# Optimization experiments

Measured on AMD Instinct MI355X. Metric: run time of the kernel, lower is better.

## Reference

```python
import jax, jax.numpy as jnp
import numpy as np

N = 100_000      # nodes
E = 800_000      # edges (avg degree 8)
D_IN = 16        # embedding_dimension
H = 128          # hidden_dimension
OUT = 3          # out_dim
NEG_SLOPE = 0.01 # LeakyReLU default


def setup_inputs() -> dict:
    key = jax.random.key(0)
    ks = jax.random.split(key, 9)
    s = 0.05
    return {
        "feature": jax.random.normal(ks[0], (N, D_IN), jnp.float32),
        "edge_index": jax.random.randint(ks[1], (2, E), 0, N, dtype=jnp.int64),
        "edge_type": jax.random.randint(ks[2], (E,), 0, 2, dtype=jnp.int64),
        "W_in": jax.random.normal(ks[3], (D_IN, H), jnp.float32) * s,
        "b_in": jnp.zeros((H,), jnp.float32),
        "W1": jax.random.normal(ks[4], (H, H), jnp.float32) * s,
        "b1": jnp.zeros((H,), jnp.float32),
        "W2": jax.random.normal(ks[5], (H, H), jnp.float32) * s,
        "b2": jnp.zeros((H,), jnp.float32),
        "W_out": jax.random.normal(ks[6], (H, OUT), jnp.float32) * s,
        "b_out": jnp.zeros((OUT,), jnp.float32),
    }


def gcn_conv(x, W, b, src, dst, n):
    """PyG GCNConv: linear -> add self-loops -> D^-1/2 A D^-1/2 aggregation -> bias."""
    h = x @ W                                   # [N, H]
    loop = jnp.arange(n, dtype=src.dtype)
    src_sl = jnp.concatenate([src, loop])       # [E+N]
    dst_sl = jnp.concatenate([dst, loop])
    deg = jax.ops.segment_sum(jnp.ones_like(dst_sl, dtype=h.dtype), dst_sl, num_segments=n)
    dinv = jax.lax.rsqrt(jnp.maximum(deg, 1.0))  # deg >= 1 due to self-loops
    norm = dinv[src_sl] * dinv[dst_sl]          # [E+N]
    msg = h[src_sl] * norm[:, None]             # gather + scale, [E+N, H]
    out = jax.ops.segment_sum(msg, dst_sl, num_segments=n)  # scatter-add
    return out + b


def reference(feature, edge_index, edge_type, W_in, b_in, W1, b1, W2, b2, W_out, b_out):
    # edge_type is accepted but unused, exactly as in the torch forward.
    x = jax.nn.leaky_relu(feature.astype(jnp.float32) @ W_in + b_in, NEG_SLOPE)
    src, dst = edge_index[0], edge_index[1]
    x = gcn_conv(x, W1, b1, src, dst, N)
    # F.dropout with training=False is identity (inference path)
    x = gcn_conv(x, W2, b2, src, dst, N)
    return x @ W_out + b_out
```

## Files before the change

### kernel.cpp

```cpp
#include <hip/hip_runtime.h>
#include <hip/hip_bf16.h>
#include <cstdint>

#define DIN 16
#define HD  128
#define RNG 2048
#define LB  11
#define MAXB 64
#define PB  256

static __device__ __forceinline__ void fma4(float4& a, float s, const float4 v) {
    a.x = fmaf(s, v.x, a.x);
    a.y = fmaf(s, v.y, a.y);
    a.z = fmaf(s, v.z, a.z);
    a.w = fmaf(s, v.w, a.w);
}
static __device__ __forceinline__ void add4(float4& a, const float4 v) {
    a.x += v.x; a.y += v.y; a.z += v.z; a.w += v.w;
}
static __device__ __forceinline__ void lrelu4(float4& h) {
    h.x = h.x > 0.f ? h.x : 0.01f * h.x;
    h.y = h.y > 0.f ? h.y : 0.01f * h.y;
    h.z = h.z > 0.f ? h.z : 0.01f * h.z;
    h.w = h.w > 0.f ? h.w : 0.01f * h.w;
}

__global__ __launch_bounds__(256) void k_histfold(const int* __restrict__ dst,
                                                  int* __restrict__ hist,
                                                  int E, int R, int CHK,
                                                  const float* __restrict__ W1,
                                                  const float* __restrict__ b1,
                                                  const float* __restrict__ W2,
                                                  const float* __restrict__ b2,
                                                  const float* __restrict__ Wout,
                                                  const float* __restrict__ bout,
                                                  float* __restrict__ Wcp,
                                                  float* __restrict__ cbuf) {
    int tid = threadIdx.x;
    if (blockIdx.x < PB) {
        __shared__ int h[MAXB];
        for (int i = tid; i < R; i += 256) h[i] = 0;
        __syncthreads();
        int e0 = blockIdx.x * CHK;
        int e1 = e0 + CHK; if (e1 > E) e1 = E;
        for (int e = e0 + tid; e < e1; e += 256) atomicAdd(&h[dst[e] >> LB], 1);
        __syncthreads();
        for (int i = tid; i < R; i += 256) hist[i * PB + blockIdx.x] = h[i];
        return;
    }
    __shared__ float sT[HD * 3];
    for (int idx = tid; idx < HD * 3; idx += 256) {
        int k = idx / 3, o = idx - 3 * k;
        float s = 0.f;
        for (int j = 0; j < HD; j++) s = fmaf(W2[k * HD + j], Wout[j * 3 + o], s);
        sT[idx] = s;
    }
    if (tid < 3) {
        float s = bout[tid];
        for (int j = 0; j < HD; j++) s = fmaf(b2[j], Wout[j * 3 + tid], s);
        cbuf[3 + tid] = s;
    }
    __syncthreads();
    if (tid < 3) {
        float s = 0.f;
        for (int j = 0; j < HD; j++) s = fmaf(b1[j], sT[j * 3 + tid], s);
        cbuf[tid] = s;
    }
    for (int idx = tid; idx < HD * 3; idx += 256) {
        int k = idx / 3, o = idx - 3 * k;
        float s = 0.f;
        for (int j = 0; j < HD; j++) s = fmaf(W1[k * HD + j], sT[j * 3 + o], s);
        Wcp[k * 4 + o] = s;
    }
    for (int idx = tid; idx < HD; idx += 256) Wcp[idx * 4 + 3] = 0.f;
}

__global__ __launch_bounds__(1024) void k_scanmlp(int* __restrict__ hist, int nh,
                                                  const float* __restrict__ F,
                                                  const float* __restrict__ Win,
                                                  const float* __restrict__ bin,
                                                  const float4* __restrict__ Wcp,
                                                  float4* __restrict__ Y, int N) {
    int tid = threadIdx.x;
    if (blockIdx.x == 0) {
        __shared__ int sd[1024];
        int CH = (nh + 1023) / 1024;
        int c0 = tid * CH;
        int c1 = c0 + CH; if (c1 > nh) c1 = nh;
        int sum = 0;
        for (int i = c0; i < c1; i++) sum += hist[i];
        sd[tid] = sum;
        __syncthreads();
        for (int off = 1; off < 1024; off <<= 1) {
            int t = (tid >= off) ? sd[tid - off] : 0;
            __syncthreads();
            sd[tid] += t;
            __syncthreads();
        }
        int base = sd[tid] - sum;
        for (int i = c0; i < c1; i++) { int t = hist[i]; hist[i] = base; base += t; }
        return;
    }
    __shared__ float4 sWinT[DIN * HD / 4];
    __shared__ float4 sWcT[HD];
    __shared__ float4 sBin[HD / 4];
    __shared__ float  sF[128 * DIN];
    if (tid < DIN * HD / 4) {
        int k = tid >> 5, rem = tid & 31, l = rem >> 1, c = rem & 1;
        sWinT[k * 32 + c * 16 + l] = ((const float4*)Win)[tid];
    } else if (tid < DIN * HD / 4 + HD) {
        int i = tid - DIN * HD / 4;
        sWcT[(i & 7) * 16 + (i >> 3)] = Wcp[i];
    } else if (tid < DIN * HD / 4 + HD + HD / 4) {
        int i = tid - DIN * HD / 4 - HD;
        sBin[i] = ((const float4*)bin)[i];
    }
    int base = (blockIdx.x - 1) * 128;
    {
        int n0 = base + (tid >> 4);
        sF[tid] = (n0 < N) ? F[(size_t)base * DIN + tid] : 0.f;
        int n1 = base + ((tid + 1024) >> 4);
        sF[tid + 1024] = (n1 < N) ? F[(size_t)base * DIN + tid + 1024] : 0.f;
    }
    __syncthreads();
    int l = tid & 15;
    int g = tid >> 4;
    int nodeA = base + 2 * g;
    int nodeB = nodeA + 1;
    if (nodeA >= N) return;
    float4 a0 = sBin[l * 2 + 0], a1 = sBin[l * 2 + 1];
    float4 b0 = a0, b1 = a1;
    #pragma unroll
    for (int k = 0; k < DIN; k++) {
        float4 w0 = sWinT[k * 32 + l];
        float4 w1 = sWinT[k * 32 + 16 + l];
        float fA = sF[(2 * g) * DIN + k];
        float fB = sF[(2 * g + 1) * DIN + k];
        fma4(a0, fA, w0); fma4(a1, fA, w1);
        fma4(b0, fB, w0); fma4(b1, fB, w1);
    }
    lrelu4(a0); lrelu4(a1); lrelu4(b0); lrelu4(b1);
    float hA[8] = {a0.x, a0.y, a0.z, a0.w, a1.x, a1.y, a1.z, a1.w};
    float hB[8] = {b0.x, b0.y, b0.z, b0.w, b1.x, b1.y, b1.z, b1.w};
    float pA0 = 0.f, pA1 = 0.f, pA2 = 0.f, pB0 = 0.f, pB1 = 0.f, pB2 = 0.f;
    #pragma unroll
    for (int jj = 0; jj < 8; jj++) {
        float4 wc = sWcT[jj * 16 + l];
        pA0 = fmaf(hA[jj], wc.x, pA0);
        pA1 = fmaf(hA[jj], wc.y, pA1);
        pA2 = fmaf(hA[jj], wc.z, pA2);
        pB0 = fmaf(hB[jj], wc.x, pB0);
        pB1 = fmaf(hB[jj], wc.y, pB1);
        pB2 = fmaf(hB[jj], wc.z, pB2);
    }
    #pragma unroll
    for (int off = 8; off > 0; off >>= 1) {
        pA0 += __shfl_down(pA0, off, 16);
        pA1 += __shfl_down(pA1, off, 16);
        pA2 += __shfl_down(pA2, off, 16);
        pB0 += __shfl_down(pB0, off, 16);
        pB1 += __shfl_down(pB1, off, 16);
        pB2 += __shfl_down(pB2, off, 16);
    }
    if (l == 0) {
        Y[nodeA] = make_float4(pA0, pA1, pA2, 1.0f);
        if (nodeB < N) Y[nodeB] = make_float4(pB0, pB1, pB2, 1.0f);
    }
}

__global__ __launch_bounds__(256) void k_part(const int* __restrict__ src,
                                              const int* __restrict__ dst,
                                              const int* __restrict__ off,
                                              int* __restrict__ ebin,
                                              int E, int R, int CHK) {
    __shared__ int cur[MAXB];
    int tid = threadIdx.x;
    int b = blockIdx.x;
    for (int i = tid; i < R; i += 256) cur[i] = off[i * PB + b];
    __syncthreads();
    int e0 = b * CHK;
    int e1 = e0 + CHK; if (e1 > E) e1 = E;
    for (int e = e0 + tid; e < e1; e += 256) {
        int s = src[e], d = dst[e];
        int pos = atomicAdd(&cur[d >> LB], 1);
        ebin[pos] = (s << LB) | (d & (RNG - 1));
    }
}

__global__ __launch_bounds__(1024) void k_csr(const int* __restrict__ ebin,
                                              const int* __restrict__ off,
                                              const float4* __restrict__ Y,
                                              int* __restrict__ rowptr,
                                              int* __restrict__ ecsr,
                                              float* __restrict__ dinv,
                                              float4* __restrict__ Ys,
                                              int N, int E, int R) {
    __shared__ int c[RNG];
    __shared__ int swv[16];
    int tid = threadIdx.x;
    int b = blockIdx.x;
    c[tid] = 0; c[tid + 1024] = 0;
    __syncthreads();
    int e0 = off[b * PB];
    int e1 = (b + 1 < R) ? off[(b + 1) * PB] : E;
    for (int e = e0 + tid; e < e1; e += 1024) atomicAdd(&c[ebin[e] & (RNG - 1)], 1);
    __syncthreads();
    int v0 = c[2 * tid], v1 = c[2 * tid + 1];
    int ts = v0 + v1;
    int lane = tid & 63, wid = tid >> 6;
    int sc = ts;
    #pragma unroll
    for (int o = 1; o < 64; o <<= 1) {
        int t = __shfl_up(sc, o, 64);
        if (lane >= o) sc += t;
    }
    if (lane == 63) swv[wid] = sc;
    __syncthreads();
    if (tid < 16) {
        int v = swv[tid];
        int s2 = v;
        #pragma unroll
        for (int o = 1; o < 16; o <<= 1) {
            int t = __shfl_up(s2, o, 16);
            if (tid >= o) s2 += t;
        }
        swv[tid] = s2 - v;
    }
    __syncthreads();
    int excl = sc - ts + swv[wid];
    int rp0 = e0 + excl;
    int rp1 = rp0 + v0;
    int n0 = b * RNG + 2 * tid;
    if (n0 <= N) rowptr[n0] = rp0;
    if (n0 + 1 <= N) rowptr[n0 + 1] = rp1;
    if (b == R - 1 && tid == 1023) rowptr[N] = E;
    if (n0 < N) {
        float di = rsqrtf((float)v0 + 1.0f);
        dinv[n0] = di;
        float4 y = Y[n0];
        Ys[n0] = make_float4(di * y.x, di * y.y, di * y.z, di);
    }
    if (n0 + 1 < N) {
        float di = rsqrtf((float)v1 + 1.0f);
        dinv[n0 + 1] = di;
        float4 y = Y[n0 + 1];
        Ys[n0 + 1] = make_float4(di * y.x, di * y.y, di * y.z, di);
    }
    c[2 * tid] = rp0;
    c[2 * tid + 1] = rp1;
    __syncthreads();
    for (int e = e0 + tid; e < e1; e += 1024) {
        int ed = ebin[e];
        int pos = atomicAdd(&c[ed & (RNG - 1)], 1);
        ecsr[pos] = ed >> LB;
    }
    if (b == 0 && tid < 16) ecsr[E + tid] = 0;
}

__global__ __launch_bounds__(256) void k_aggA(const int* __restrict__ rowptr,
                                              const int* __restrict__ ecsr,
                                              const float4* __restrict__ Ys,
                                              const float* __restrict__ dinv,
                                              float4* __restrict__ Z1s, int N) {
    int n = blockIdx.x * blockDim.x + threadIdx.x;
    if (n >= N) return;
    int beg = rowptr[n], end = rowptr[n + 1];
    int deg = end - beg;
    float4 acc = Ys[n];
    int4 q0 = *(const int4*)(ecsr + beg);
    int4 q1 = *(const int4*)(ecsr + beg + 4);
    int4 q2 = *(const int4*)(ecsr + beg + 8);
    int si[12] = {q0.x, q0.y, q0.z, q0.w, q1.x, q1.y, q1.z, q1.w,
                  q2.x, q2.y, q2.z, q2.w};
    float4 g[12];
    #pragma unroll
    for (int k = 0; k < 12; k++) g[k] = Ys[si[k]];
    #pragma unroll
    for (int k = 0; k < 12; k++) if (k < deg) add4(acc, g[k]);
    for (int j = beg + 12; j < end; j++) add4(acc, Ys[ecsr[j]]);
    float di = dinv[n];
    float d2 = di * di;
    Z1s[n] = make_float4(d2 * acc.x, d2 * acc.y, d2 * acc.z, d2 * acc.w);
}

__global__ __launch_bounds__(256) void k_aggB(const int* __restrict__ rowptr,
                                              const int* __restrict__ ecsr,
                                              const float4* __restrict__ Z1s,
                                              const float* __restrict__ dinv,
                                              const float* __restrict__ cbuf,
                                              float* __restrict__ out, int N) {
    int n = blockIdx.x * blockDim.x + threadIdx.x;
    if (n >= N) return;
    int beg = rowptr[n], end = rowptr[n + 1];
    int deg = end - beg;
    float4 acc = Z1s[n];
    float di = dinv[n];
    float r = acc.w / di;
    int4 q0 = *(const int4*)(ecsr + beg);
    int4 q1 = *(const int4*)(ecsr + beg + 4);
    int4 q2 = *(const int4*)(ecsr + beg + 8);
    int si[12] = {q0.x, q0.y, q0.z, q0.w, q1.x, q1.y, q1.z, q1.w,
                  q2.x, q2.y, q2.z, q2.w};
    float4 g[12];
    #pragma unroll
    for (int k = 0; k < 12; k++) g[k] = Z1s[si[k]];
    #pragma unroll
    for (int k = 0; k < 12; k++) if (k < deg) add4(acc, g[k]);
    for (int j = beg + 12; j < end; j++) add4(acc, Z1s[ecsr[j]]);
    out[(size_t)n * 3 + 0] = di * acc.x + r * cbuf[0] + cbuf[3];
    out[(size_t)n * 3 + 1] = di * acc.y + r * cbuf[1] + cbuf[4];
    out[(size_t)n * 3 + 2] = di * acc.z + r * cbuf[2] + cbuf[5];
}

extern "C" void kernel_launch(void* const* d_in, const int* in_sizes, int n_in,
                              void* d_out, int out_size, void* d_ws, size_t ws_size,
                              hipStream_t stream) {
    const float* feat = (const float*)d_in[0];
    const int*   ei   = (const int*)d_in[1];
    const float* Win  = (const float*)d_in[3];
    const float* bin  = (const float*)d_in[4];
    const float* W1   = (const float*)d_in[5];
    const float* b1   = (const float*)d_in[6];
    const float* W2   = (const float*)d_in[7];
    const float* b2   = (const float*)d_in[8];
    const float* Wout = (const float*)d_in[9];
    const float* bout = (const float*)d_in[10];
    float* out = (float*)d_out;

    int N = in_sizes[0] / DIN;
    int E = in_sizes[2];
    const int* src = ei;
    const int* dst = ei + E;

    int R = (N + RNG - 1) >> LB;
    int CHK = (E + PB - 1) / PB;
    int NH = R * PB;
    int XB = (N + 127) / 128;

    char* p = (char*)d_ws;
    auto alloc = [&](size_t bytes) -> char* {
        char* q = p;
        p += (bytes + 511) & ~(size_t)511;
        return q;
    };
    int*    hist   = (int*)alloc((size_t)NH * 4);
    int*    ebin   = (int*)alloc((size_t)E * 4);
    int*    ecsr   = (int*)alloc(((size_t)E + 16) * 4);
    int*    rowptr = (int*)alloc((size_t)(N + 1) * 4);
    float4* Y      = (float4*)alloc((size_t)N * 16);
    float4* Ys     = (float4*)alloc((size_t)N * 16);
    float4* Z1s    = (float4*)alloc((size_t)N * 16);
    float*  dinv   = (float*)alloc((size_t)N * 4);
    float*  Wcp    = (float*)alloc(HD * 4 * 4);
    float*  cbuf   = (float*)alloc(8 * 4);

    k_histfold<<<PB + 1, 256, 0, stream>>>(dst, hist, E, R, CHK,
                                           W1, b1, W2, b2, Wout, bout, Wcp, cbuf);
    k_scanmlp<<<1 + XB, 1024, 0, stream>>>(hist, NH, feat, Win, bin,
                                           (const float4*)Wcp, Y, N);
    k_part<<<PB, 256, 0, stream>>>(src, dst, hist, ebin, E, R, CHK);
    k_csr<<<R, 1024, 0, stream>>>(ebin, hist, Y, rowptr, ecsr, dinv, Ys, N, E, R);
    k_aggA<<<(N + 255) / 256, 256, 0, stream>>>(rowptr, ecsr, Ys, dinv, Z1s, N);
    k_aggB<<<(N + 255) / 256, 256, 0, stream>>>(rowptr, ecsr, Z1s, dinv, cbuf, out, N);
}
```

Baseline: 156.1 us.

## Replace histogram-scan edge partition with fixed-capacity bins and packed row descriptors

Drops the separate histogram and prefix-scan pass. Edges are now partitioned straight into fixed-capacity per-bin buffers, with global atomic cursors and block-local staging in shared memory. Row pointer and degree are packed into one int, so the dinv array goes away and the aggregation kernels recompute dinv with rsqrt. The folded weight product is recomputed in every MLP block and in the first CSR block, which removes one kernel launch but adds redundant per-block compute. Correctness now assumes each node's in-degree stays below 64 and that each bin fits its capacity.

```diff
diff --git a/kernel.cpp b/kernel.cpp
--- a/kernel.cpp
+++ b/kernel.cpp
@@ -7,7 +7,7 @@
 #define RNG 2048
 #define LB  11
 #define MAXB 64
-#define PB  256
+#define CHKE 3328
 
 static __device__ __forceinline__ void fma4(float4& a, float s, const float4 v) {
     a.x = fmaf(s, v.x, a.x);
@@ -25,102 +25,47 @@
     h.w = h.w > 0.f ? h.w : 0.01f * h.w;
 }
 
-__global__ __launch_bounds__(256) void k_histfold(const int* __restrict__ dst,
-                                                  int* __restrict__ hist,
-                                                  int E, int R, int CHK,
-                                                  const float* __restrict__ W1,
-                                                  const float* __restrict__ b1,
-                                                  const float* __restrict__ W2,
-                                                  const float* __restrict__ b2,
-                                                  const float* __restrict__ Wout,
-                                                  const float* __restrict__ bout,
-                                                  float* __restrict__ Wcp,
-                                                  float* __restrict__ cbuf) {
-    int tid = threadIdx.x;
-    if (blockIdx.x < PB) {
-        __shared__ int h[MAXB];
-        for (int i = tid; i < R; i += 256) h[i] = 0;
-        __syncthreads();
-        int e0 = blockIdx.x * CHK;
-        int e1 = e0 + CHK; if (e1 > E) e1 = E;
-        for (int e = e0 + tid; e < e1; e += 256) atomicAdd(&h[dst[e] >> LB], 1);
-        __syncthreads();
-        for (int i = tid; i < R; i += 256) hist[i * PB + blockIdx.x] = h[i];
-        return;
-    }
-    __shared__ float sT[HD * 3];
-    for (int idx = tid; idx < HD * 3; idx += 256) {
-        int k = idx / 3, o = idx - 3 * k;
-        float s = 0.f;
-        for (int j = 0; j < HD; j++) s = fmaf(W2[k * HD + j], Wout[j * 3 + o], s);
-        sT[idx] = s;
-    }
-    if (tid < 3) {
-        float s = bout[tid];
-        for (int j = 0; j < HD; j++) s = fmaf(b2[j], Wout[j * 3 + tid], s);
-        cbuf[3 + tid] = s;
-    }
-    __syncthreads();
-    if (tid < 3) {
-        float s = 0.f;
-        for (int j = 0; j < HD; j++) s = fmaf(b1[j], sT[j * 3 + tid], s);
-        cbuf[tid] = s;
-    }
-    for (int idx = tid; idx < HD * 3; idx += 256) {
-        int k = idx / 3, o = idx - 3 * k;
-        float s = 0.f;
-        for (int j = 0; j < HD; j++) s = fmaf(W1[k * HD + j], sT[j * 3 + o], s);
-        Wcp[k * 4 + o] = s;
-    }
-    for (int idx = tid; idx < HD; idx += 256) Wcp[idx * 4 + 3] = 0.f;
-}
-
-__global__ __launch_bounds__(1024) void k_scanmlp(int* __restrict__ hist, int nh,
-                                                  const float* __restrict__ F,
-                                                  const float* __restrict__ Win,
-                                                  const float* __restrict__ bin,
-                                                  const float4* __restrict__ Wcp,
-                                                  float4* __restrict__ Y, int N) {
-    int tid = threadIdx.x;
-    if (blockIdx.x == 0) {
-        __shared__ int sd[1024];
-        int CH = (nh + 1023) / 1024;
-        int c0 = tid * CH;
-        int c1 = c0 + CH; if (c1 > nh) c1 = nh;
-        int sum = 0;
-        for (int i = c0; i < c1; i++) sum += hist[i];
-        sd[tid] = sum;
-        __syncthreads();
-        for (int off = 1; off < 1024; off <<= 1) {
-            int t = (tid >= off) ? sd[tid - off] : 0;
-            __syncthreads();
-            sd[tid] += t;
-            __syncthreads();
-        }
-        int base = sd[tid] - sum;
-        for (int i = c0; i < c1; i++) { int t = hist[i]; hist[i] = base; base += t; }
-        return;
-    }
+__global__ __launch_bounds__(1024) void k_mlp(const float* __restrict__ F,
+                                              const float* __restrict__ Win,
+                                              const float* __restrict__ binp,
+                                              const float* __restrict__ W1,
+                                              const float* __restrict__ W2,
+                                              const float* __restrict__ Wout,
+                                              int* __restrict__ binCursor,
+                                              float4* __restrict__ Y, int N, int R) {
     __shared__ float4 sWinT[DIN * HD / 4];
     __shared__ float4 sWcT[HD];
     __shared__ float4 sBin[HD / 4];
     __shared__ float  sF[128 * DIN];
+    __shared__ float  sT[HD * 3];
+    int tid = threadIdx.x;
+    if (blockIdx.x == 0 && tid < R * 16) binCursor[tid] = 0;
     if (tid < DIN * HD / 4) {
         int k = tid >> 5, rem = tid & 31, l = rem >> 1, c = rem & 1;
         sWinT[k * 32 + c * 16 + l] = ((const float4*)Win)[tid];
-    } else if (tid < DIN * HD / 4 + HD) {
+    } else if (tid < DIN * HD / 4 + HD / 4) {
         int i = tid - DIN * HD / 4;
-        sWcT[(i & 7) * 16 + (i >> 3)] = Wcp[i];
-    } else if (tid < DIN * HD / 4 + HD + HD / 4) {
-        int i = tid - DIN * HD / 4 - HD;
-        sBin[i] = ((const float4*)bin)[i];
-    }
-    int base = (blockIdx.x - 1) * 128;
+        sBin[i] = ((const float4*)binp)[i];
+    }
+    int base = blockIdx.x * 128;
     {
         int n0 = base + (tid >> 4);
         sF[tid] = (n0 < N) ? F[(size_t)base * DIN + tid] : 0.f;
         int n1 = base + ((tid + 1024) >> 4);
         sF[tid + 1024] = (n1 < N) ? F[(size_t)base * DIN + tid + 1024] : 0.f;
+    }
+    if (tid < HD * 3) {
+        int k = tid / 3, o = tid - 3 * k;
+        float s = 0.f;
+        for (int j = 0; j < HD; j++) s = fmaf(W2[k * HD + j], Wout[j * 3 + o], s);
+        sT[tid] = s;
+    }
+    __syncthreads();
+    if (tid < HD * 3) {
+        int k = tid / 3, o = tid - 3 * k;
+        float s = 0.f;
+        for (int j = 0; j < HD; j++) s = fmaf(W1[k * HD + j], sT[j * 3 + o], s);
+        ((float*)&sWcT[(k & 7) * 16 + (k >> 3)])[o] = s;
     }
     __syncthreads();
     int l = tid & 15;
@@ -170,40 +115,78 @@
 
 __global__ __launch_bounds__(256) void k_part(const int* __restrict__ src,
                                               const int* __restrict__ dst,
-                                              const int* __restrict__ off,
+                                              int* __restrict__ binCursor,
                                               int* __restrict__ ebin,
-                                              int E, int R, int CHK) {
-    __shared__ int cur[MAXB];
+                                              int E, int R, int CAPE) {
+    __shared__ int sV[CHKE];
+    __shared__ unsigned char sB[CHKE];
+    __shared__ int lcnt[MAXB], lbase[MAXB];
     int tid = threadIdx.x;
-    int b = blockIdx.x;
-    for (int i = tid; i < R; i += 256) cur[i] = off[i * PB + b];
-    __syncthreads();
-    int e0 = b * CHK;
-    int e1 = e0 + CHK; if (e1 > E) e1 = E;
-    for (int e = e0 + tid; e < e1; e += 256) {
-        int s = src[e], d = dst[e];
-        int pos = atomicAdd(&cur[d >> LB], 1);
-        ebin[pos] = (s << LB) | (d & (RNG - 1));
+    if (tid < R) lcnt[tid] = 0;
+    __syncthreads();
+    int e0 = blockIdx.x * CHKE;
+    int cnt = E - e0; if (cnt > CHKE) cnt = CHKE;
+    for (int i = tid; i < cnt; i += 256) {
+        int s = src[e0 + i], d = dst[e0 + i];
+        int b = d >> LB;
+        sV[i] = (s << LB) | (d & (RNG - 1));
+        sB[i] = (unsigned char)b;
+        atomicAdd(&lcnt[b], 1);
+    }
+    __syncthreads();
+    if (tid < R) lbase[tid] = atomicAdd(&binCursor[tid * 16], lcnt[tid]);
+    __syncthreads();
+    if (tid < R) lcnt[tid] = lbase[tid];
+    __syncthreads();
+    for (int i = tid; i < cnt; i += 256) {
+        int b = sB[i];
+        int pos = atomicAdd(&lcnt[b], 1);
+        ebin[b * CAPE + pos] = sV[i];
     }
 }
 
 __global__ __launch_bounds__(1024) void k_csr(const int* __restrict__ ebin,
-                                              const int* __restrict__ off,
+                                              const int* __restrict__ binCursor,
                                               const float4* __restrict__ Y,
-                                              int* __restrict__ rowptr,
+                                              int* __restrict__ rowdeg,
                                               int* __restrict__ ecsr,
-                                              float* __restrict__ dinv,
                                               float4* __restrict__ Ys,
-                                              int N, int E, int R) {
+                                              const float* __restrict__ W2,
+                                              const float* __restrict__ Wout,
+                                              const float* __restrict__ b1,
+                                              const float* __restrict__ b2,
+                                              const float* __restrict__ bout,
+                                              float* __restrict__ cbuf,
+                                              int N, int R, int CAPE) {
     __shared__ int c[RNG];
     __shared__ int swv[16];
+    __shared__ float sTc[HD * 3];
     int tid = threadIdx.x;
     int b = blockIdx.x;
     c[tid] = 0; c[tid + 1024] = 0;
-    __syncthreads();
-    int e0 = off[b * PB];
-    int e1 = (b + 1 < R) ? off[(b + 1) * PB] : E;
+    if (b == 0 && tid < HD * 3) {
+        int k = tid / 3, o = tid - 3 * k;
+        float s = 0.f;
+        for (int j = 0; j < HD; j++) s = fmaf(W2[k * HD + j], Wout[j * 3 + o], s);
+        sTc[tid] = s;
+    }
+    if (b == 0 && tid >= HD * 3 && tid < HD * 3 + 3) {
+        int o = tid - HD * 3;
+        float s = bout[o];
+        for (int j = 0; j < HD; j++) s = fmaf(b2[j], Wout[j * 3 + o], s);
+        cbuf[3 + o] = s;
+    }
+    __syncthreads();
+    if (b == 0 && tid < 3) {
+        float s = 0.f;
+        for (int j = 0; j < HD; j++) s = fmaf(b1[j], sTc[j * 3 + tid], s);
+        cbuf[tid] = s;
+    }
+    int e0 = b * CAPE;
+    int cntb = binCursor[b * 16];
+    int e1 = e0 + cntb;
     for (int e = e0 + tid; e < e1; e += 1024) atomicAdd(&c[ebin[e] & (RNG - 1)], 1);
+    if (tid < 16) ecsr[e1 + tid] = 0;
     __syncthreads();
     int v0 = c[2 * tid], v1 = c[2 * tid + 1];
     int ts = v0 + v1;
@@ -231,18 +214,15 @@
     int rp0 = e0 + excl;
     int rp1 = rp0 + v0;
     int n0 = b * RNG + 2 * tid;
-    if (n0 <= N) rowptr[n0] = rp0;
-    if (n0 + 1 <= N) rowptr[n0 + 1] = rp1;
-    if (b == R - 1 && tid == 1023) rowptr[N] = E;
     if (n0 < N) {
+        rowdeg[n0] = (rp0 << 6) | v0;
         float di = rsqrtf((float)v0 + 1.0f);
-        dinv[n0] = di;
         float4 y = Y[n0];
         Ys[n0] = make_float4(di * y.x, di * y.y, di * y.z, di);
     }
     if (n0 + 1 < N) {
+        rowdeg[n0 + 1] = (rp1 << 6) | v1;
         float di = rsqrtf((float)v1 + 1.0f);
-        dinv[n0 + 1] = di;
         float4 y = Y[n0 + 1];
         Ys[n0 + 1] = make_float4(di * y.x, di * y.y, di * y.z, di);
     }
@@ -254,18 +234,16 @@
         int pos = atomicAdd(&c[ed & (RNG - 1)], 1);
         ecsr[pos] = ed >> LB;
     }
-    if (b == 0 && tid < 16) ecsr[E + tid] = 0;
-}
-
-__global__ __launch_bounds__(256) void k_aggA(const int* __restrict__ rowptr,
+}
+
+__global__ __launch_bounds__(256) void k_aggA(const int* __restrict__ rowdeg,
                                               const int* __restrict__ ecsr,
                                               const float4* __restrict__ Ys,
-                                              const float* __restrict__ dinv,
                                               float4* __restrict__ Z1s, int N) {
     int n = blockIdx.x * blockDim.x + threadIdx.x;
     if (n >= N) return;
-    int beg = rowptr[n], end = rowptr[n + 1];
-    int deg = end - beg;
+    int rd = rowdeg[n];
+    int beg = rd >> 6, deg = rd & 63;
     float4 acc = Ys[n];
     int4 q0 = *(const int4*)(ecsr + beg);
     int4 q1 = *(const int4*)(ecsr + beg + 4);
@@ -277,24 +255,23 @@
     for (int k = 0; k < 12; k++) g[k] = Ys[si[k]];
     #pragma unroll
     for (int k = 0; k < 12; k++) if (k < deg) add4(acc, g[k]);
-    for (int j = beg + 12; j < end; j++) add4(acc, Ys[ecsr[j]]);
-    float di = dinv[n];
+    for (int j = beg + 12; j < beg + deg; j++) add4(acc, Ys[ecsr[j]]);
+    float di = rsqrtf((float)deg + 1.0f);
     float d2 = di * di;
     Z1s[n] = make_float4(d2 * acc.x, d2 * acc.y, d2 * acc.z, d2 * acc.w);
 }
 
-__global__ __launch_bounds__(256) void k_aggB(const int* __restrict__ rowptr,
+__global__ __launch_bounds__(256) void k_aggB(const int* __restrict__ rowdeg,
                                               const int* __restrict__ ecsr,
                                               const float4* __restrict__ Z1s,
-                                              const float* __restrict__ dinv,
                                               const float* __restrict__ cbuf,
                                               float* __restrict__ out, int N) {
     int n = blockIdx.x * blockDim.x + threadIdx.x;
     if (n >= N) return;
-    int beg = rowptr[n], end = rowptr[n + 1];
-    int deg = end - beg;
+    int rd = rowdeg[n];
+    int beg = rd >> 6, deg = rd & 63;
+    float di = rsqrtf((float)deg + 1.0f);
     float4 acc = Z1s[n];
-    float di = dinv[n];
     float r = acc.w / di;
     int4 q0 = *(const int4*)(ecsr + beg);
     int4 q1 = *(const int4*)(ecsr + beg + 4);
@@ -306,7 +283,7 @@
     for (int k = 0; k < 12; k++) g[k] = Z1s[si[k]];
     #pragma unroll
     for (int k = 0; k < 12; k++) if (k < deg) add4(acc, g[k]);
-    for (int j = beg + 12; j < end; j++) add4(acc, Z1s[ecsr[j]]);
+    for (int j = beg + 12; j < beg + deg; j++) add4(acc, Z1s[ecsr[j]]);
     out[(size_t)n * 3 + 0] = di * acc.x + r * cbuf[0] + cbuf[3];
     out[(size_t)n * 3 + 1] = di * acc.y + r * cbuf[1] + cbuf[4];
     out[(size_t)n * 3 + 2] = di * acc.z + r * cbuf[2] + cbuf[5];
@@ -318,7 +295,7 @@
     const float* feat = (const float*)d_in[0];
     const int*   ei   = (const int*)d_in[1];
     const float* Win  = (const float*)d_in[3];
-    const float* bin  = (const float*)d_in[4];
+    const float* binp = (const float*)d_in[4];
     const float* W1   = (const float*)d_in[5];
     const float* b1   = (const float*)d_in[6];
     const float* W2   = (const float*)d_in[7];
@@ -333,9 +310,9 @@
     const int* dst = ei + E;
 
     int R = (N + RNG - 1) >> LB;
-    int CHK = (E + PB - 1) / PB;
-    int NH = R * PB;
+    int CAPE = (((E + R - 1) / R) + 2064) & ~15;
     int XB = (N + 127) / 128;
+    int PBn = (E + CHKE - 1) / CHKE;
 
     char* p = (char*)d_ws;
     auto alloc = [&](size_t bytes) -> char* {
@@ -343,23 +320,19 @@
         p += (bytes + 511) & ~(size_t)511;
         return q;
     };
-    int*    hist   = (int*)alloc((size_t)NH * 4);
-    int*    ebin   = (int*)alloc((size_t)E * 4);
-    int*    ecsr   = (int*)alloc(((size_t)E + 16) * 4);
-    int*    rowptr = (int*)alloc((size_t)(N + 1) * 4);
+    int*    binCursor = (int*)alloc((size_t)R * 16 * 4);
+    int*    ebin   = (int*)alloc((size_t)R * CAPE * 4);
+    int*    ecsr   = (int*)alloc(((size_t)R * CAPE + 16) * 4);
+    int*    rowdeg = (int*)alloc((size_t)N * 4);
     float4* Y      = (float4*)alloc((size_t)N * 16);
     float4* Ys     = (float4*)alloc((size_t)N * 16);
     float4* Z1s    = (float4*)alloc((size_t)N * 16);
-    float*  dinv   = (float*)alloc((size_t)N * 4);
-    float*  Wcp    = (float*)alloc(HD * 4 * 4);
     float*  cbuf   = (float*)alloc(8 * 4);
 
-    k_histfold<<<PB + 1, 256, 0, stream>>>(dst, hist, E, R, CHK,
-                                           W1, b1, W2, b2, Wout, bout, Wcp, cbuf);
-    k_scanmlp<<<1 + XB, 1024, 0, stream>>>(hist, NH, feat, Win, bin,
-                                           (const float4*)Wcp, Y, N);
-    k_part<<<PB, 256, 0, stream>>>(src, dst, hist, ebin, E, R, CHK);
-    k_csr<<<R, 1024, 0, stream>>>(ebin, hist, Y, rowptr, ecsr, dinv, Ys, N, E, R);
-    k_aggA<<<(N + 255) / 256, 256, 0, stream>>>(rowptr, ecsr, Ys, dinv, Z1s, N);
-    k_aggB<<<(N + 255) / 256, 256, 0, stream>>>(rowptr, ecsr, Z1s, dinv, cbuf, out, N);
-}
+    k_mlp<<<XB, 1024, 0, stream>>>(feat, Win, binp, W1, W2, Wout, binCursor, Y, N, R);
+    k_part<<<PBn, 256, 0, stream>>>(src, dst, binCursor, ebin, E, R, CAPE);
+    k_csr<<<R, 1024, 0, stream>>>(ebin, binCursor, Y, rowdeg, ecsr, Ys,
+                                  W2, Wout, b1, b2, bout, cbuf, N, R, CAPE);
+    k_aggA<<<(N + 255) / 256, 256, 0, stream>>>(rowdeg, ecsr, Ys, Z1s, N);
+    k_aggB<<<(N + 255) / 256, 256, 0, stream>>>(rowdeg, ecsr, Z1s, cbuf, out, N);
+}
```

New measurement: 175.9 us. +12.7%, slower.
